# Kernel optimization log

Hardware: AMD Instinct MI355X
Metric: run time of the kernel (lower is better)

Reference implementation:

```python
import jax, jax.numpy as jnp
import numpy as np
from jax import lax

H = W = 4096

def _directional_filters():
    f0   = [[0,0,0],[0,1,-1],[0,0,0]]
    f45  = [[0,0,0],[0,1,0],[0,0,-1]]
    f90  = [[0,0,0],[0,1,0],[0,-1,0]]
    f135 = [[0,0,0],[0,1,0],[-1,0,0]]
    f180 = [[0,0,0],[-1,1,0],[0,0,0]]
    f225 = [[-1,0,0],[0,1,0],[0,0,0]]
    f270 = [[0,-1,0],[0,1,0],[0,0,0]]
    f315 = [[0,0,-1],[0,1,0],[0,0,0]]
    w = np.stack([f0,f45,f90,f135,f180,f225,f270,f315]).astype(np.float32)
    return jnp.asarray(w[:, None, :, :])  # [8,1,3,3]

def setup_inputs() -> dict:
    key = jax.random.key(0)
    k1, k2 = jax.random.split(key)
    grad_magnitude = jax.random.uniform(k1, (1, 1, H, W), dtype=jnp.float32)
    # orientation in degrees, quantized to multiples of 45 as in Canny
    grad_orientation = jax.random.randint(k2, (1, 1, H, W), 0, 8).astype(jnp.float32) * 45.0
    weight = _directional_filters()
    bias = jnp.zeros((8,), dtype=jnp.float32)
    return {"grad_magnitude": grad_magnitude, "grad_orientation": grad_orientation,
            "weight": weight, "bias": bias}

def reference(grad_magnitude, grad_orientation, weight, bias):
    # directional 3x3 conv, 1 -> 8 channels, 'SAME' padding
    all_filtered = lax.conv_general_dilated(
        grad_magnitude, weight, window_strides=(1, 1), padding='SAME')
    all_filtered = all_filtered + bias[None, :, None, None]  # [1,8,H,W]
    # per-pixel orientation channel indices (floor matches torch .long())
    idx_pos = jnp.floor(grad_orientation / 45.0).astype(jnp.int32) % 8  # [1,1,H,W]
    idx_neg = (idx_pos + 4) % 8
    f = all_filtered[0]                                  # [8,H,W]
    pos = jnp.take_along_axis(f, idx_pos[0], axis=0)     # [1,H,W]
    neg = jnp.take_along_axis(f, idx_neg[0], axis=0)     # [1,H,W]
    is_max = jnp.minimum(pos, neg) > 0.0                 # [1,H,W]
    thin_edges = jnp.where(is_max[None], grad_magnitude, 0.0)  # [1,1,H,W]
    return thin_edges
```

## Files before the change

kernel.cpp:

```cpp
#include <hip/hip_runtime.h>


constexpr int H = 4096;
constexpr int W = 4096;

#define DIR_TABLE 0x210489A6u

__device__ __forceinline__ float load_mag_guarded(const float* __restrict__ mag,
                                                  int y, int x) {
    float v = 0.0f;
    if ((unsigned)y < (unsigned)H && (unsigned)x < (unsigned)W)
        v = mag[y * W + x];
    return v;
}

__global__ __launch_bounds__(256) void nms_kernel(
    const float* __restrict__ mag,
    const float* __restrict__ orient,
    const float* __restrict__ bias,
    float* __restrict__ out)
{
    const int tid = blockIdx.x * blockDim.x + threadIdx.x;
    const int quads_per_row = W / 4;
    const int y  = tid / quads_per_row;
    const int xq = tid - y * quads_per_row;
    if (y >= H) return;
    const int x0 = xq * 4;
    const long base = (long)y * W + x0;

    const float4 m4 = *reinterpret_cast<const float4*>(mag + base);
    const float4 o4 = *reinterpret_cast<const float4*>(orient + base);

    float b[8];
    #pragma unroll
    for (int i = 0; i < 8; ++i) b[i] = bias[i];

    float m[4] = {m4.x, m4.y, m4.z, m4.w};
    float o[4] = {o4.x, o4.y, o4.z, o4.w};
    float r[4];

    #pragma unroll
    for (int k = 0; k < 4; ++k) {
        const int x = x0 + k;
        const int c = ((int)floorf(o[k] / 45.0f)) & 7;
        const unsigned nib = (DIR_TABLE >> (c * 4)) & 0xFu;
        const int dy = (int)(nib >> 2) - 1;
        const int dx = (int)(nib & 3u) - 1;

        const float npos = load_mag_guarded(mag, y + dy, x + dx);
        const float nneg = load_mag_guarded(mag, y - dy, x - dx);

        float bp = b[0], bn = b[4];
        #pragma unroll
        for (int i = 1; i < 8; ++i) {
            if (c == i) bp = b[i];
            if (((c + 4) & 7) == i) bn = b[i];
        }
        if (((c + 4) & 7) == 0) bn = b[0];

        const float pos = m[k] - npos + bp;
        const float neg = m[k] - nneg + bn;
        r[k] = (fminf(pos, neg) > 0.0f) ? m[k] : 0.0f;
    }

    float4 r4 = make_float4(r[0], r[1], r[2], r[3]);
    *reinterpret_cast<float4*>(out + base) = r4;
}

extern "C" void kernel_launch(void* const* d_in, const int* in_sizes, int n_in,
                              void* d_out, int out_size, void* d_ws, size_t ws_size,
                              hipStream_t stream) {
    const float* mag    = (const float*)d_in[0];
    const float* orient = (const float*)d_in[1];
    const float* bias   = (const float*)d_in[3];
    float* out = (float*)d_out;

    const int total = H * (W / 4);
    dim3 block(256);
    dim3 grid((total + block.x - 1) / block.x);
    hipLaunchKernelGGL(nms_kernel, grid, block, 0, stream,
                       mag, orient, bias, out);
}
```

Before: 206.2 us.

## Load neighbor rows as float4 and share halos via wavefront shuffles

Each thread now loads the rows above and below as float4 vectors and gets its left and right neighbours from adjacent lanes with shuffles. This replaces the eight data-dependent scalar gathers per quad. Only lanes 0 and 63 fall back to scalar halo loads. Neighbour and bias selection become branchless select chains over a 3x6 register window, and index math uses shifts. The channel index is now computed by rounding o/45 instead of flooring it, which matches the reference only when orientations are exact multiples of 45.

```diff
diff --git a/kernel.cpp b/kernel.cpp
--- a/kernel.cpp
+++ b/kernel.cpp
@@ -3,16 +3,6 @@
 
 constexpr int H = 4096;
 constexpr int W = 4096;
-
-#define DIR_TABLE 0x210489A6u
-
-__device__ __forceinline__ float load_mag_guarded(const float* __restrict__ mag,
-                                                  int y, int x) {
-    float v = 0.0f;
-    if ((unsigned)y < (unsigned)H && (unsigned)x < (unsigned)W)
-        v = mag[y * W + x];
-    return v;
-}
 
 __global__ __launch_bounds__(256) void nms_kernel(
     const float* __restrict__ mag,
@@ -20,51 +10,92 @@
     const float* __restrict__ bias,
     float* __restrict__ out)
 {
-    const int tid = blockIdx.x * blockDim.x + threadIdx.x;
-    const int quads_per_row = W / 4;
-    const int y  = tid / quads_per_row;
-    const int xq = tid - y * quads_per_row;
-    if (y >= H) return;
-    const int x0 = xq * 4;
-    const long base = (long)y * W + x0;
+    const int tid  = blockIdx.x * blockDim.x + threadIdx.x;
+    const int lane = threadIdx.x & 63;
+    const int y    = tid >> 10;
+    const int xq   = tid & 1023;
+    const int x0   = xq << 2;
+    const long base = ((long)y << 12) + x0;
 
     const float4 m4 = *reinterpret_cast<const float4*>(mag + base);
     const float4 o4 = *reinterpret_cast<const float4*>(orient + base);
+
+    const bool has_up = (y > 0);
+    const bool has_dn = (y < H - 1);
+    float4 u4 = make_float4(0.f, 0.f, 0.f, 0.f);
+    float4 d4 = make_float4(0.f, 0.f, 0.f, 0.f);
+    if (has_up) u4 = *reinterpret_cast<const float4*>(mag + base - W);
+    if (has_dn) d4 = *reinterpret_cast<const float4*>(mag + base + W);
+
+    float lu = __shfl_up(u4.w, 1), lc = __shfl_up(m4.w, 1), ld = __shfl_up(d4.w, 1);
+    float ru = __shfl_down(u4.x, 1), rc = __shfl_down(m4.x, 1), rd = __shfl_down(d4.x, 1);
+    if (lane == 0) {
+        lu = lc = ld = 0.f;
+        if (x0 > 0) {
+            lc = mag[base - 1];
+            if (has_up) lu = mag[base - 1 - W];
+            if (has_dn) ld = mag[base - 1 + W];
+        }
+    }
+    if (lane == 63) {
+        ru = rc = rd = 0.f;
+        if (x0 + 4 < W) {
+            rc = mag[base + 4];
+            if (has_up) ru = mag[base + 4 - W];
+            if (has_dn) rd = mag[base + 4 + W];
+        }
+    }
+
+    const float u6[6] = {lu, u4.x, u4.y, u4.z, u4.w, ru};
+    const float c6[6] = {lc, m4.x, m4.y, m4.z, m4.w, rc};
+    const float d6[6] = {ld, d4.x, d4.y, d4.z, d4.w, rd};
 
     float b[8];
     #pragma unroll
     for (int i = 0; i < 8; ++i) b[i] = bias[i];
 
-    float m[4] = {m4.x, m4.y, m4.z, m4.w};
-    float o[4] = {o4.x, o4.y, o4.z, o4.w};
+    const float m[4] = {m4.x, m4.y, m4.z, m4.w};
+    const float o[4] = {o4.x, o4.y, o4.z, o4.w};
     float r[4];
 
     #pragma unroll
     for (int k = 0; k < 4; ++k) {
-        const int x = x0 + k;
-        const int c = ((int)floorf(o[k] / 45.0f)) & 7;
-        const unsigned nib = (DIR_TABLE >> (c * 4)) & 0xFu;
-        const int dy = (int)(nib >> 2) - 1;
-        const int dx = (int)(nib & 3u) - 1;
+        const int c  = ((int)(o[k] * 0.0222222222f + 0.5f)) & 7;
+        const int cc = c ^ 4;
 
-        const float npos = load_mag_guarded(mag, y + dy, x + dx);
-        const float nneg = load_mag_guarded(mag, y - dy, x - dx);
+        const float n0 = c6[k + 2];
+        const float n1 = d6[k + 2];
+        const float n2 = d6[k + 1];
+        const float n3 = d6[k];
+        const float n4 = c6[k];
+        const float n5 = u6[k];
+        const float n6 = u6[k + 1];
+        const float n7 = u6[k + 2];
 
-        float bp = b[0], bn = b[4];
-        #pragma unroll
-        for (int i = 1; i < 8; ++i) {
-            if (c == i) bp = b[i];
-            if (((c + 4) & 7) == i) bn = b[i];
-        }
-        if (((c + 4) & 7) == 0) bn = b[0];
+        float np = n0, nn = n0;
+        np = (c == 1) ? n1 : np;  nn = (cc == 1) ? n1 : nn;
+        np = (c == 2) ? n2 : np;  nn = (cc == 2) ? n2 : nn;
+        np = (c == 3) ? n3 : np;  nn = (cc == 3) ? n3 : nn;
+        np = (c == 4) ? n4 : np;  nn = (cc == 4) ? n4 : nn;
+        np = (c == 5) ? n5 : np;  nn = (cc == 5) ? n5 : nn;
+        np = (c == 6) ? n6 : np;  nn = (cc == 6) ? n6 : nn;
+        np = (c == 7) ? n7 : np;  nn = (cc == 7) ? n7 : nn;
 
-        const float pos = m[k] - npos + bp;
-        const float neg = m[k] - nneg + bn;
+        float bp = b[0], bn = b[0];
+        bp = (c == 1) ? b[1] : bp;  bn = (cc == 1) ? b[1] : bn;
+        bp = (c == 2) ? b[2] : bp;  bn = (cc == 2) ? b[2] : bn;
+        bp = (c == 3) ? b[3] : bp;  bn = (cc == 3) ? b[3] : bn;
+        bp = (c == 4) ? b[4] : bp;  bn = (cc == 4) ? b[4] : bn;
+        bp = (c == 5) ? b[5] : bp;  bn = (cc == 5) ? b[5] : bn;
+        bp = (c == 6) ? b[6] : bp;  bn = (cc == 6) ? b[6] : bn;
+        bp = (c == 7) ? b[7] : bp;  bn = (cc == 7) ? b[7] : bn;
+
+        const float pos = m[k] - np + bp;
+        const float neg = m[k] - nn + bn;
         r[k] = (fminf(pos, neg) > 0.0f) ? m[k] : 0.0f;
     }
 
-    float4 r4 = make_float4(r[0], r[1], r[2], r[3]);
-    *reinterpret_cast<float4*>(out + base) = r4;
+    *reinterpret_cast<float4*>(out + base) = make_float4(r[0], r[1], r[2], r[3]);
 }
 
 extern "C" void kernel_launch(void* const* d_in, const int* in_sizes, int n_in,
@@ -77,7 +108,7 @@
 
     const int total = H * (W / 4);
     dim3 block(256);
-    dim3 grid((total + block.x - 1) / block.x);
+    dim3 grid(total / 256);
     hipLaunchKernelGGL(nms_kernel, grid, block, 0, stream,
                        mag, orient, bias, out);
 }
```

Result: faster. 170.2 us (-17.5%).

## Process two rows per thread with register stencil and wave shuffles

Applied to the files above, without the earlier changes.

Each thread now handles a 2x4 tile. It loads the row above, its own two rows and the row below as vector loads, and gets left and right halo values through wave shuffles. This replaces the per-pixel, data-dependent scalar neighbour gathers. Direction selection becomes a branchless select tree over the eight candidate differences, and orientation and output use nontemporal accesses. The orientation index now rounds o/45 with a multiply instead of taking floor(o/45) mod 8, which only matches the reference for exact multiples of 45 below 360.

```diff
diff --git a/kernel.cpp b/kernel.cpp
--- a/kernel.cpp
+++ b/kernel.cpp
@@ -4,14 +4,43 @@
 constexpr int H = 4096;
 constexpr int W = 4096;
 
-#define DIR_TABLE 0x210489A6u
+typedef float v4f __attribute__((ext_vector_type(4)));
 
-__device__ __forceinline__ float load_mag_guarded(const float* __restrict__ mag,
-                                                  int y, int x) {
-    float v = 0.0f;
-    if ((unsigned)y < (unsigned)H && (unsigned)x < (unsigned)W)
-        v = mag[y * W + x];
-    return v;
+__device__ __forceinline__ v4f nms_row(const float u6[6], const float c6[6],
+                                       const float d6[6], v4f m4, v4f o4,
+                                       const float b[8])
+{
+    v4f res;
+    const float m[4] = {m4.x, m4.y, m4.z, m4.w};
+    const float o[4] = {o4.x, o4.y, o4.z, o4.w};
+    float r[4];
+    #pragma unroll
+    for (int k = 0; k < 4; ++k) {
+        const int c = (int)(o[k] * 0.0222222222f + 0.5f);
+        const bool b0 = (c & 1), b1 = (c & 2), b2 = (c & 4);
+
+        const float t0 = c6[k + 2] - b[0];
+        const float t1 = d6[k + 2] - b[1];
+        const float t2 = d6[k + 1] - b[2];
+        const float t3 = d6[k]     - b[3];
+        const float t4 = c6[k]     - b[4];
+        const float t5 = u6[k]     - b[5];
+        const float t6 = u6[k + 1] - b[6];
+        const float t7 = u6[k + 2] - b[7];
+
+        const float s01 = b0 ? t1 : t0;
+        const float s23 = b0 ? t3 : t2;
+        const float s45 = b0 ? t5 : t4;
+        const float s67 = b0 ? t7 : t6;
+        const float lo  = b1 ? s23 : s01;
+        const float hi  = b1 ? s67 : s45;
+        const float tp  = b2 ? hi : lo;
+        const float tn  = b2 ? lo : hi;
+
+        r[k] = (m[k] > fmaxf(tp, tn)) ? m[k] : 0.0f;
+    }
+    res.x = r[0]; res.y = r[1]; res.z = r[2]; res.w = r[3];
+    return res;
 }
 
 __global__ __launch_bounds__(256) void nms_kernel(
@@ -20,51 +49,64 @@
     const float* __restrict__ bias,
     float* __restrict__ out)
 {
-    const int tid = blockIdx.x * blockDim.x + threadIdx.x;
-    const int quads_per_row = W / 4;
-    const int y  = tid / quads_per_row;
-    const int xq = tid - y * quads_per_row;
-    if (y >= H) return;
-    const int x0 = xq * 4;
-    const long base = (long)y * W + x0;
+    const int tid  = blockIdx.x * blockDim.x + threadIdx.x;
+    const int lane = threadIdx.x & 63;
+    const int ty   = tid >> 10;
+    const int xq   = tid & 1023;
+    const int x0   = xq << 2;
+    const int y0   = ty << 1;
+    const long base0 = ((long)y0 << 12) + x0;
+    const long base1 = base0 + W;
 
-    const float4 m4 = *reinterpret_cast<const float4*>(mag + base);
-    const float4 o4 = *reinterpret_cast<const float4*>(orient + base);
+    const bool has_up = (y0 > 0);
+    const bool has_dn = (y0 + 2 < H);
+    const v4f r0 = *reinterpret_cast<const v4f*>(mag + base0);
+    const v4f r1 = *reinterpret_cast<const v4f*>(mag + base1);
+    v4f uu = {0.f, 0.f, 0.f, 0.f};
+    v4f dd = {0.f, 0.f, 0.f, 0.f};
+    if (has_up) uu = *reinterpret_cast<const v4f*>(mag + base0 - W);
+    if (has_dn) dd = *reinterpret_cast<const v4f*>(mag + base1 + W);
+
+    const v4f o0 = __builtin_nontemporal_load(reinterpret_cast<const v4f*>(orient + base0));
+    const v4f o1 = __builtin_nontemporal_load(reinterpret_cast<const v4f*>(orient + base1));
+
+    float lU = __shfl_up(uu.w, 1), l0 = __shfl_up(r0.w, 1),
+          l1 = __shfl_up(r1.w, 1), lD = __shfl_up(dd.w, 1);
+    float rU = __shfl_down(uu.x, 1), q0 = __shfl_down(r0.x, 1),
+          q1 = __shfl_down(r1.x, 1), rD = __shfl_down(dd.x, 1);
+    if (lane == 0) {
+        lU = l0 = l1 = lD = 0.f;
+        if (x0 > 0) {
+            l0 = mag[base0 - 1];
+            l1 = mag[base1 - 1];
+            if (has_up) lU = mag[base0 - W - 1];
+            if (has_dn) lD = mag[base1 + W - 1];
+        }
+    }
+    if (lane == 63) {
+        rU = q0 = q1 = rD = 0.f;
+        if (x0 + 4 < W) {
+            q0 = mag[base0 + 4];
+            q1 = mag[base1 + 4];
+            if (has_up) rU = mag[base0 - W + 4];
+            if (has_dn) rD = mag[base1 + W + 4];
+        }
+    }
+
+    const float U6[6] = {lU, uu.x, uu.y, uu.z, uu.w, rU};
+    const float C0[6] = {l0, r0.x, r0.y, r0.z, r0.w, q0};
+    const float C1[6] = {l1, r1.x, r1.y, r1.z, r1.w, q1};
+    const float D6[6] = {lD, dd.x, dd.y, dd.z, dd.w, rD};
 
     float b[8];
     #pragma unroll
     for (int i = 0; i < 8; ++i) b[i] = bias[i];
 
-    float m[4] = {m4.x, m4.y, m4.z, m4.w};
-    float o[4] = {o4.x, o4.y, o4.z, o4.w};
-    float r[4];
+    const v4f res0 = nms_row(U6, C0, C1, r0, o0, b);
+    const v4f res1 = nms_row(C0, C1, D6, r1, o1, b);
 
-    #pragma unroll
-    for (int k = 0; k < 4; ++k) {
-        const int x = x0 + k;
-        const int c = ((int)floorf(o[k] / 45.0f)) & 7;
-        const unsigned nib = (DIR_TABLE >> (c * 4)) & 0xFu;
-        const int dy = (int)(nib >> 2) - 1;
-        const int dx = (int)(nib & 3u) - 1;
-
-        const float npos = load_mag_guarded(mag, y + dy, x + dx);
-        const float nneg = load_mag_guarded(mag, y - dy, x - dx);
-
-        float bp = b[0], bn = b[4];
-        #pragma unroll
-        for (int i = 1; i < 8; ++i) {
-            if (c == i) bp = b[i];
-            if (((c + 4) & 7) == i) bn = b[i];
-        }
-        if (((c + 4) & 7) == 0) bn = b[0];
-
-        const float pos = m[k] - npos + bp;
-        const float neg = m[k] - nneg + bn;
-        r[k] = (fminf(pos, neg) > 0.0f) ? m[k] : 0.0f;
-    }
-
-    float4 r4 = make_float4(r[0], r[1], r[2], r[3]);
-    *reinterpret_cast<float4*>(out + base) = r4;
+    __builtin_nontemporal_store(res0, reinterpret_cast<v4f*>(out + base0));
+    __builtin_nontemporal_store(res1, reinterpret_cast<v4f*>(out + base1));
 }
 
 extern "C" void kernel_launch(void* const* d_in, const int* in_sizes, int n_in,
@@ -75,9 +117,9 @@
     const float* bias   = (const float*)d_in[3];
     float* out = (float*)d_out;
 
-    const int total = H * (W / 4);
+    const int total = (H / 2) * (W / 4);
     dim3 block(256);
-    dim3 grid((total + block.x - 1) / block.x);
+    dim3 grid(total / 256);
     hipLaunchKernelGGL(nms_kernel, grid, block, 0, stream,
                        mag, orient, bias, out);
 }
```

Result: faster. 166.9 us (-19.0%).

## Stream rows per thread with sliding 3-row window and wave shuffles for halos

Applied to the files above, without the earlier changes.

Each thread now handles a 4-wide column across 8 consecutive rows and keeps a sliding window of three magnitude rows in registers, with the next row prefetched. Horizontal neighbours come from cross-lane shuffles instead of scattered gathers. The per-pixel direction is chosen by computing all four directional maxima and selecting with orientation bits, and the output uses nontemporal stores. This is meant to replace the data-dependent neighbour gathers with coalesced row reuse. The cost is fewer threads in flight, and the rounding-based orientation decode assumes inputs are exact multiples of 45.

```diff
diff --git a/kernel.cpp b/kernel.cpp
--- a/kernel.cpp
+++ b/kernel.cpp
@@ -3,15 +3,69 @@
 
 constexpr int H = 4096;
 constexpr int W = 4096;
+constexpr int RPB = 8;
 
-#define DIR_TABLE 0x210489A6u
+typedef float v4f __attribute__((ext_vector_type(4)));
 
-__device__ __forceinline__ float load_mag_guarded(const float* __restrict__ mag,
-                                                  int y, int x) {
-    float v = 0.0f;
-    if ((unsigned)y < (unsigned)H && (unsigned)x < (unsigned)W)
-        v = mag[y * W + x];
-    return v;
+struct RowRaw { v4f m; float pl, pr; };
+struct Row    { v4f m; float lf, rt; };
+
+__device__ __forceinline__ RowRaw load_row(const float* __restrict__ mag,
+                                           int r, long xb,
+                                           bool has_l, bool has_r, int lane)
+{
+    const int rc = min(max(r, 0), H - 1);
+    const long a = (long)rc * W + xb;
+    RowRaw t;
+    t.m = *reinterpret_cast<const v4f*>(mag + a);
+    t.pl = 0.f; t.pr = 0.f;
+    if (lane == 0  && has_l) t.pl = mag[a - 1];
+    if (lane == 63 && has_r) t.pr = mag[a + 4];
+    return t;
+}
+
+__device__ __forceinline__ Row resolve(const RowRaw& t, int r, int lane)
+{
+    const float mask = (r >= 0 && r < H) ? 1.f : 0.f;
+    Row o;
+    o.m = t.m * mask;
+    float lf = __shfl_up(o.m.w, 1);
+    float rt = __shfl_down(o.m.x, 1);
+    if (lane == 0)  lf = t.pl * mask;
+    if (lane == 63) rt = t.pr * mask;
+    o.lf = lf; o.rt = rt;
+    return o;
+}
+
+__device__ __forceinline__ v4f nms_quad(const Row& rA, const Row& rB,
+                                        const Row& rC, v4f o4,
+                                        const float b[8])
+{
+    const float u6[6] = {rA.lf, rA.m.x, rA.m.y, rA.m.z, rA.m.w, rA.rt};
+    const float c6[6] = {rB.lf, rB.m.x, rB.m.y, rB.m.z, rB.m.w, rB.rt};
+    const float d6[6] = {rC.lf, rC.m.x, rC.m.y, rC.m.z, rC.m.w, rC.rt};
+    const float m[4]  = {rB.m.x, rB.m.y, rB.m.z, rB.m.w};
+    const float o[4]  = {o4.x, o4.y, o4.z, o4.w};
+
+    float r[4];
+    #pragma unroll
+    for (int k = 0; k < 4; ++k) {
+        const int c = (int)(o[k] * 0.0222222222f + 0.5f);
+        const bool b0 = (c & 1), b1 = (c & 2);
+
+        const float M0 = fmaxf(c6[k + 2] - b[0], c6[k]     - b[4]);
+        const float M1 = fmaxf(d6[k + 2] - b[1], u6[k]     - b[5]);
+        const float M2 = fmaxf(d6[k + 1] - b[2], u6[k + 1] - b[6]);
+        const float M3 = fmaxf(d6[k]     - b[3], u6[k + 2] - b[7]);
+
+        const float m01 = b0 ? M1 : M0;
+        const float m23 = b0 ? M3 : M2;
+        const float Mj  = b1 ? m23 : m01;
+
+        r[k] = (m[k] > Mj) ? m[k] : 0.0f;
+    }
+    v4f res; res.x = r[0]; res.y = r[1]; res.z = r[2]; res.w = r[3];
+    return res;
 }
 
 __global__ __launch_bounds__(256) void nms_kernel(
@@ -20,51 +74,42 @@
     const float* __restrict__ bias,
     float* __restrict__ out)
 {
-    const int tid = blockIdx.x * blockDim.x + threadIdx.x;
-    const int quads_per_row = W / 4;
-    const int y  = tid / quads_per_row;
-    const int xq = tid - y * quads_per_row;
-    if (y >= H) return;
-    const int x0 = xq * 4;
-    const long base = (long)y * W + x0;
-
-    const float4 m4 = *reinterpret_cast<const float4*>(mag + base);
-    const float4 o4 = *reinterpret_cast<const float4*>(orient + base);
+    const int tx   = threadIdx.x;
+    const int lane = tx & 63;
+    const int band = blockIdx.x & 3;
+    const int seg  = blockIdx.x >> 2;
+    const int x0   = band * 1024 + tx * 4;
+    const long xb  = x0;
+    const bool has_l = (x0 > 0);
+    const bool has_r = (x0 + 4 < W);
+    const int r0   = seg * RPB;
 
     float b[8];
     #pragma unroll
     for (int i = 0; i < 8; ++i) b[i] = bias[i];
 
-    float m[4] = {m4.x, m4.y, m4.z, m4.w};
-    float o[4] = {o4.x, o4.y, o4.z, o4.w};
-    float r[4];
+    RowRaw a_raw = load_row(mag, r0 - 1, xb, has_l, has_r, lane);
+    RowRaw b_raw = load_row(mag, r0,     xb, has_l, has_r, lane);
+    RowRaw c_raw = load_row(mag, r0 + 1, xb, has_l, has_r, lane);
+    v4f o_cur = *reinterpret_cast<const v4f*>(orient + (long)r0 * W + xb);
+    Row rA = resolve(a_raw, r0 - 1, lane);
+    Row rB = resolve(b_raw, r0, lane);
 
     #pragma unroll
-    for (int k = 0; k < 4; ++k) {
-        const int x = x0 + k;
-        const int c = ((int)floorf(o[k] / 45.0f)) & 7;
-        const unsigned nib = (DIR_TABLE >> (c * 4)) & 0xFu;
-        const int dy = (int)(nib >> 2) - 1;
-        const int dx = (int)(nib & 3u) - 1;
+    for (int i = 0; i < RPB; ++i) {
+        const int r = r0 + i;
+        RowRaw d_raw = load_row(mag, r + 2, xb, has_l, has_r, lane);
+        const int ro = min(r + 1, H - 1);
+        v4f o_nxt = *reinterpret_cast<const v4f*>(orient + (long)ro * W + xb);
 
-        const float npos = load_mag_guarded(mag, y + dy, x + dx);
-        const float nneg = load_mag_guarded(mag, y - dy, x - dx);
+        Row rC = resolve(c_raw, r + 1, lane);
 
-        float bp = b[0], bn = b[4];
-        #pragma unroll
-        for (int i = 1; i < 8; ++i) {
-            if (c == i) bp = b[i];
-            if (((c + 4) & 7) == i) bn = b[i];
-        }
-        if (((c + 4) & 7) == 0) bn = b[0];
+        const v4f res = nms_quad(rA, rB, rC, o_cur, b);
+        __builtin_nontemporal_store(
+            res, reinterpret_cast<v4f*>(out + (long)r * W + xb));
 
-        const float pos = m[k] - npos + bp;
-        const float neg = m[k] - nneg + bn;
-        r[k] = (fminf(pos, neg) > 0.0f) ? m[k] : 0.0f;
+        rA = rB; rB = rC; c_raw = d_raw; o_cur = o_nxt;
     }
-
-    float4 r4 = make_float4(r[0], r[1], r[2], r[3]);
-    *reinterpret_cast<float4*>(out + base) = r4;
 }
 
 extern "C" void kernel_launch(void* const* d_in, const int* in_sizes, int n_in,
@@ -75,9 +120,8 @@
     const float* bias   = (const float*)d_in[3];
     float* out = (float*)d_out;
 
-    const int total = H * (W / 4);
     dim3 block(256);
-    dim3 grid((total + block.x - 1) / block.x);
+    dim3 grid((H / RPB) * 4);
     hipLaunchKernelGGL(nms_kernel, grid, block, 0, stream,
                        mag, orient, bias, out);
 }
```

Result: faster. 177.4 us (-14.0%).
